# Performance work log

Hardware: AMD Instinct MI355X
Metric: run time of the kernel (lower is better)

Reference implementation:

```python
import jax, jax.numpy as jnp
import numpy as np

LD, LU, N, D_IN, D_OUT, K = 16384, 65536, 8, 256, 128, 3


def setup_inputs() -> dict:
    key = jax.random.key(0)
    ks = jax.random.split(key, 7)
    down_features = jax.random.normal(ks[0], (LD, N, D_IN), dtype=jnp.float32)
    up_features = jax.random.normal(ks[1], (LU, N, D_OUT), dtype=jnp.float32)
    idx = jax.random.randint(ks[2], (LU, N, K), 0, LD, dtype=jnp.int32)
    W1 = jax.random.normal(ks[3], (D_IN, D_OUT), dtype=jnp.float32) / np.sqrt(D_IN)
    b1 = jnp.zeros((D_OUT,), dtype=jnp.float32)
    W2 = jax.random.normal(ks[4], (D_OUT, D_OUT), dtype=jnp.float32) / np.sqrt(D_OUT)
    b2 = jnp.zeros((D_OUT,), dtype=jnp.float32)
    return {"down_features": down_features, "up_features": up_features, "idx": idx,
            "W1": W1, "b1": b1, "W2": W2, "b2": b2}


def reference(down_features, up_features, idx, W1, b1, W2, b2):
    # MLP: Linear(d, d_out) -> ReLU -> Linear(d_out, d_out), applied per point
    h = jax.nn.relu(jnp.einsum("lnd,de->lne", down_features, W1) + b1)
    h = jnp.einsum("lnd,de->lne", h, W2) + b2            # (Ld, N, Du)
    # KNN upsample: gather K neighbors per upsampled point, average, residual add
    n = jnp.arange(h.shape[1])[None, :, None]            # (1, N, 1) batch index
    gathered = h[idx, n, :]                              # (Lu, N, K, Du)
    up = up_features + gathered.mean(axis=2)             # (Lu, N, Du)
    return up
```

## Files before the change

kernel.cpp:

```cpp
#include <hip/hip_runtime.h>

#define LD_   16384
#define LU_   65536
#define N_    8
#define DIN   256
#define DOUT  128
#define K_    3
#define M_    (LD_ * N_)

typedef short bf16x8 __attribute__((ext_vector_type(8)));
typedef float f32x4  __attribute__((ext_vector_type(4)));

__device__ __forceinline__ unsigned short f2bf(float f) {
    unsigned int x = __float_as_uint(f);
    x += 0x7fffu + ((x >> 16) & 1u);
    return (unsigned short)(x >> 16);
}

__device__ __forceinline__ bf16x8 ld_bf16x8(const unsigned short* p) {
    const short4 lo = *(const short4*)p;
    const short4 hi = *(const short4*)(p + 4);
    bf16x8 r = {lo.x, lo.y, lo.z, lo.w, hi.x, hi.y, hi.z, hi.w};
    return r;
}

#define W1_STRIDE 264
#define W2_STRIDE 132
#define H1_STRIDE 132

__global__ __launch_bounds__(512, 2) void knn_mlp_mfma(
    const float* __restrict__ down, const float* __restrict__ W1,
    const float* __restrict__ b1,   const float* __restrict__ W2,
    const float* __restrict__ b2,   unsigned short* __restrict__ h)
{
    __shared__ unsigned short sW1t[DOUT * W1_STRIDE];
    __shared__ unsigned short sW2t[DOUT * W2_STRIDE];
    __shared__ unsigned short sH[8][16 * H1_STRIDE];

    const int tid = threadIdx.x;

    #pragma unroll
    for (int it = 0; it < 16; ++it) {
        const int fid = it * 512 + tid;
        const int k = fid >> 5, n4 = (fid & 31) * 4;
        const float4 w = ((const float4*)W1)[fid];
        sW1t[(n4 + 0) * W1_STRIDE + k] = f2bf(w.x);
        sW1t[(n4 + 1) * W1_STRIDE + k] = f2bf(w.y);
        sW1t[(n4 + 2) * W1_STRIDE + k] = f2bf(w.z);
        sW1t[(n4 + 3) * W1_STRIDE + k] = f2bf(w.w);
    }
    #pragma unroll
    for (int it = 0; it < 8; ++it) {
        const int fid = it * 512 + tid;
        const int k = fid >> 5, n4 = (fid & 31) * 4;
        const float4 w = ((const float4*)W2)[fid];
        sW2t[(n4 + 0) * W2_STRIDE + k] = f2bf(w.x);
        sW2t[(n4 + 1) * W2_STRIDE + k] = f2bf(w.y);
        sW2t[(n4 + 2) * W2_STRIDE + k] = f2bf(w.z);
        sW2t[(n4 + 3) * W2_STRIDE + k] = f2bf(w.w);
    }
    __syncthreads();

    const int wave = tid >> 6, lane = tid & 63;
    const int lm = lane & 15, lg = lane >> 4;
    unsigned short* hw = sH[wave];

    float b1r[8], b2r[8];
    #pragma unroll
    for (int nt = 0; nt < 8; ++nt) {
        b1r[nt] = b1[nt * 16 + lm];
        b2r[nt] = b2[nt * 16 + lm];
    }

    const int row0 = blockIdx.x * 512 + wave * 16;
    const float* dbase = down + (size_t)(row0 + lm) * DIN + lg * 8;

    float4 raw[2][16];

    #pragma unroll
    for (int k = 0; k < 8; ++k) {
        raw[0][2 * k]     = *(const float4*)(dbase + k * 32);
        raw[0][2 * k + 1] = *(const float4*)(dbase + k * 32 + 4);
    }

    #pragma unroll
    for (int pass = 0; pass < 4; ++pass) {
        const int cur = pass & 1;
        const int chunk = row0 + pass * 128;

        if (pass < 3) {
            const float* dp = dbase + (size_t)(pass + 1) * 128 * DIN;
            #pragma unroll
            for (int k = 0; k < 8; ++k) {
                raw[cur ^ 1][2 * k]     = *(const float4*)(dp + k * 32);
                raw[cur ^ 1][2 * k + 1] = *(const float4*)(dp + k * 32 + 4);
            }
        }

        f32x4 acc[8];
        #pragma unroll
        for (int nt = 0; nt < 8; ++nt) acc[nt] = (f32x4){0.f, 0.f, 0.f, 0.f};
        #pragma unroll
        for (int k = 0; k < 8; ++k) {
            const float4 r0 = raw[cur][2 * k], r1 = raw[cur][2 * k + 1];
            const bf16x8 a = {(short)f2bf(r0.x), (short)f2bf(r0.y), (short)f2bf(r0.z), (short)f2bf(r0.w),
                              (short)f2bf(r1.x), (short)f2bf(r1.y), (short)f2bf(r1.z), (short)f2bf(r1.w)};
            const int koff = k * 32 + lg * 8;
            #pragma unroll
            for (int nt = 0; nt < 8; ++nt) {
                const bf16x8 B = ld_bf16x8(&sW1t[(nt * 16 + lm) * W1_STRIDE + koff]);
                acc[nt] = __builtin_amdgcn_mfma_f32_16x16x32_bf16(a, B, acc[nt], 0, 0, 0);
            }
        }

        #pragma unroll
        for (int nt = 0; nt < 8; ++nt) {
            #pragma unroll
            for (int i = 0; i < 4; ++i) {
                float v = acc[nt][i] + b1r[nt];
                v = fmaxf(v, 0.0f);
                hw[(lg * 4 + i) * H1_STRIDE + nt * 16 + lm] = f2bf(v);
            }
        }
        asm volatile("s_waitcnt lgkmcnt(0)" ::: "memory");

        f32x4 acc2[8];
        #pragma unroll
        for (int nt = 0; nt < 8; ++nt) acc2[nt] = (f32x4){0.f, 0.f, 0.f, 0.f};
        #pragma unroll
        for (int k = 0; k < 4; ++k) {
            const int koff = k * 32 + lg * 8;
            const bf16x8 A2 = ld_bf16x8(&hw[lm * H1_STRIDE + koff]);
            #pragma unroll
            for (int nt = 0; nt < 8; ++nt) {
                const bf16x8 B = ld_bf16x8(&sW2t[(nt * 16 + lm) * W2_STRIDE + koff]);
                acc2[nt] = __builtin_amdgcn_mfma_f32_16x16x32_bf16(A2, B, acc2[nt], 0, 0, 0);
            }
        }

        #pragma unroll
        for (int nt = 0; nt < 8; ++nt) {
            #pragma unroll
            for (int i = 0; i < 4; ++i) {
                const float v = acc2[nt][i] + b2r[nt];
                h[(size_t)(chunk + lg * 4 + i) * DOUT + nt * 16 + lm] = f2bf(v);
            }
        }
    }
}

__global__ __launch_bounds__(256) void knn_gather(
    const float* __restrict__ up, const int* __restrict__ idx,
    const unsigned int* __restrict__ h32, float* __restrict__ out)
{
    const int wave = threadIdx.x >> 6, lane = threadIdx.x & 63;
    const long long wid  = (long long)blockIdx.x * 4 + wave;
    const long long base = wid * 64;

    for (int p0 = 0; p0 < 64; p0 += 4) {
        const long long pair0 = base + p0;
        const int4* ip = (const int4*)(idx + pair0 * 3);
        const int4 q0 = ip[0], q1 = ip[1], q2 = ip[2];
        const int id[4][3] = {{q0.x, q0.y, q0.z}, {q0.w, q1.x, q1.y},
                              {q1.z, q1.w, q2.x}, {q2.y, q2.z, q2.w}};

        unsigned int ga[4][3];
        float2 uu[4];
        #pragma unroll
        for (int u = 0; u < 4; ++u) {
            const long long pair = pair0 + u;
            const int n = (int)(pair & 7);
            ga[u][0] = h32[((size_t)id[u][0] * 8 + n) * 64 + lane];
            ga[u][1] = h32[((size_t)id[u][1] * 8 + n) * 64 + lane];
            ga[u][2] = h32[((size_t)id[u][2] * 8 + n) * 64 + lane];
            uu[u] = ((const float2*)up)[pair * 64 + lane];
        }
        #pragma unroll
        for (int u = 0; u < 4; ++u) {
            float sx = 0.f, sy = 0.f;
            #pragma unroll
            for (int j = 0; j < 3; ++j) {
                const unsigned int v = ga[u][j];
                sx += __uint_as_float(v << 16);
                sy += __uint_as_float(v & 0xffff0000u);
            }
            float2 o;
            o.x = uu[u].x + sx * (1.0f / 3.0f);
            o.y = uu[u].y + sy * (1.0f / 3.0f);
            ((float2*)out)[(pair0 + u) * 64 + lane] = o;
        }
    }
}

extern "C" void kernel_launch(void* const* d_in, const int* in_sizes, int n_in,
                              void* d_out, int out_size, void* d_ws, size_t ws_size,
                              hipStream_t stream)
{
    const float* down = (const float*)d_in[0];
    const float* up   = (const float*)d_in[1];
    const int*   idx  = (const int*)d_in[2];
    const float* W1   = (const float*)d_in[3];
    const float* b1   = (const float*)d_in[4];
    const float* W2   = (const float*)d_in[5];
    const float* b2   = (const float*)d_in[6];
    float* out = (float*)d_out;
    unsigned short* h = (unsigned short*)d_ws;

    knn_mlp_mfma<<<256, 512, 0, stream>>>(down, W1, b1, W2, b2, h);
    knn_gather<<<2048, 256, 0, stream>>>(up, idx, (const unsigned int*)h, out);
}
```

Before: 577.6 us.

## Widen gather kernel accesses, shuffle-broadcast indices, and use nontemporal streaming

The gather kernel now has each half-wave handle one point, so each lane loads 8 bytes of h and 16 bytes of up and out instead of 4 and 8. Each lane loads its own point's neighbour indices once, and they are broadcast with __shfl instead of every lane reloading them. The streaming up and out accesses use nontemporal load and store hints so they do not push the reused h table out of cache. The outer loop is fully unrolled into 8 groups of 4 points, which raises register use.

```diff
diff --git a/kernel.cpp b/kernel.cpp
--- a/kernel.cpp
+++ b/kernel.cpp
@@ -10,6 +10,7 @@
 
 typedef short bf16x8 __attribute__((ext_vector_type(8)));
 typedef float f32x4  __attribute__((ext_vector_type(4)));
+typedef unsigned int u32x2 __attribute__((ext_vector_type(2)));
 
 __device__ __forceinline__ unsigned short f2bf(float f) {
     unsigned int x = __float_as_uint(f);
@@ -154,40 +155,52 @@
     const unsigned int* __restrict__ h32, float* __restrict__ out)
 {
     const int wave = threadIdx.x >> 6, lane = threadIdx.x & 63;
+    const int half = lane >> 5, lih = lane & 31;
     const long long wid  = (long long)blockIdx.x * 4 + wave;
     const long long base = wid * 64;
 
-    for (int p0 = 0; p0 < 64; p0 += 4) {
-        const long long pair0 = base + p0;
-        const int4* ip = (const int4*)(idx + pair0 * 3);
-        const int4 q0 = ip[0], q1 = ip[1], q2 = ip[2];
-        const int id[4][3] = {{q0.x, q0.y, q0.z}, {q0.w, q1.x, q1.y},
-                              {q1.z, q1.w, q2.x}, {q2.y, q2.z, q2.w}};
-
-        unsigned int ga[4][3];
-        float2 uu[4];
+    const int* ip = idx + (base + lane) * 3;
+    const int mi0 = ip[0], mi1 = ip[1], mi2 = ip[2];
+
+    const u32x2* hg   = (const u32x2*)h32;
+    const f32x4* upv  = (const f32x4*)up;
+    f32x4*       outv = (f32x4*)out;
+
+    #pragma unroll
+    for (int gb = 0; gb < 8; ++gb) {
+        u32x2 ga[4][3];
+        f32x4 uu[4];
+        int   pp[4];
         #pragma unroll
         for (int u = 0; u < 4; ++u) {
-            const long long pair = pair0 + u;
-            const int n = (int)(pair & 7);
-            ga[u][0] = h32[((size_t)id[u][0] * 8 + n) * 64 + lane];
-            ga[u][1] = h32[((size_t)id[u][1] * 8 + n) * 64 + lane];
-            ga[u][2] = h32[((size_t)id[u][2] * 8 + n) * 64 + lane];
-            uu[u] = ((const float2*)up)[pair * 64 + lane];
+            const int p = (gb * 4 + u) * 2 + half;
+            pp[u] = p;
+            const int i0 = __shfl(mi0, p);
+            const int i1 = __shfl(mi1, p);
+            const int i2 = __shfl(mi2, p);
+            const int n  = p & 7;
+            ga[u][0] = hg[(unsigned)(i0 * 8 + n) * 32u + lih];
+            ga[u][1] = hg[(unsigned)(i1 * 8 + n) * 32u + lih];
+            ga[u][2] = hg[(unsigned)(i2 * 8 + n) * 32u + lih];
+            uu[u] = __builtin_nontemporal_load(&upv[(base + p) * 32 + lih]);
         }
         #pragma unroll
         for (int u = 0; u < 4; ++u) {
-            float sx = 0.f, sy = 0.f;
+            float s0 = 0.f, s1 = 0.f, s2 = 0.f, s3 = 0.f;
             #pragma unroll
             for (int j = 0; j < 3; ++j) {
-                const unsigned int v = ga[u][j];
-                sx += __uint_as_float(v << 16);
-                sy += __uint_as_float(v & 0xffff0000u);
-            }
-            float2 o;
-            o.x = uu[u].x + sx * (1.0f / 3.0f);
-            o.y = uu[u].y + sy * (1.0f / 3.0f);
-            ((float2*)out)[(pair0 + u) * 64 + lane] = o;
+                const u32x2 v = ga[u][j];
+                s0 += __uint_as_float(v.x << 16);
+                s1 += __uint_as_float(v.x & 0xffff0000u);
+                s2 += __uint_as_float(v.y << 16);
+                s3 += __uint_as_float(v.y & 0xffff0000u);
+            }
+            f32x4 o;
+            o.x = uu[u].x + s0 * (1.0f / 3.0f);
+            o.y = uu[u].y + s1 * (1.0f / 3.0f);
+            o.z = uu[u].z + s2 * (1.0f / 3.0f);
+            o.w = uu[u].w + s3 * (1.0f / 3.0f);
+            __builtin_nontemporal_store(o, &outv[(base + pp[u]) * 32 + lih]);
         }
     }
 }
```

Result: faster. 563.0 us (-2.5%).
